# Optimization experiments

Hardware: AMD Instinct MI355X
Metric: run time of the kernel (lower is better)

The kernel has to match this reference:

```python
import jax, jax.numpy as jnp
import numpy as np
from jax import lax

D_MODEL = 512
D_STATE = 16
D_CONV = 4
EXPAND = 2
D_INNER = EXPAND * D_MODEL
DT_RANK = (D_MODEL + 15) // 16  # 32


def _mamba_dir(x, in_w, conv_w, conv_b, xproj_w, dt_w, dt_b, A_log, D, out_w):
    # x: (B, L, d_model)
    B, L, _ = x.shape
    xz = jnp.einsum('bld,ed->ble', x, in_w)          # (B, L, 2*d_inner)
    xi, z = jnp.split(xz, 2, axis=-1)                # each (B, L, d_inner)
    # causal depthwise conv over time
    xc = xi.transpose(0, 2, 1)                       # (B, d_inner, L)
    xc = lax.conv_general_dilated(
        xc, conv_w, window_strides=(1,), padding=[(D_CONV - 1, 0)],
        feature_group_count=D_INNER, dimension_numbers=('NCH', 'OIH', 'NCH'))
    xi = jax.nn.silu(xc + conv_b[None, :, None]).transpose(0, 2, 1)  # (B, L, d_inner)
    # input-dependent SSM params
    x_dbl = jnp.einsum('bld,ed->ble', xi, xproj_w)   # (B, L, dt_rank + 2*d_state)
    dt, Bc, Cc = jnp.split(x_dbl, [DT_RANK, DT_RANK + D_STATE], axis=-1)
    delta = jax.nn.softplus(jnp.einsum('blr,dr->bld', dt, dt_w) + dt_b)  # (B, L, d_inner)
    A = -jnp.exp(A_log)                              # (d_inner, d_state)
    deltaA = jnp.exp(delta[..., None] * A)           # (B, L, d_inner, d_state)
    dBx = delta[..., None] * Bc[:, :, None, :] * xi[..., None]  # (B, L, d_inner, d_state)

    def step(h, inputs):
        dA_t, dBx_t, C_t = inputs
        h = dA_t * h + dBx_t                         # (B, d_inner, d_state)
        y = jnp.einsum('bdn,bn->bd', h, C_t)
        return h, y

    h0 = jnp.zeros((B, D_INNER, D_STATE), dtype=x.dtype)
    _, ys = lax.scan(step, h0,
                     (deltaA.transpose(1, 0, 2, 3),
                      dBx.transpose(1, 0, 2, 3),
                      Cc.transpose(1, 0, 2)))
    y = ys.transpose(1, 0, 2)                        # (B, L, d_inner)
    y = y + xi * D
    y = y * jax.nn.silu(z)
    return jnp.einsum('ble,de->bld', y, out_w)       # (B, L, d_model)


def _forward(x, f_in_w, f_conv_w, f_conv_b, f_xproj_w, f_dt_w, f_dt_b, f_A_log, f_D, f_out_w,
             b_in_w, b_conv_w, b_conv_b, b_xproj_w, b_dt_w, b_dt_b, b_A_log, b_D, b_out_w,
             fusion_w, fusion_b, ln_g, ln_b):
    out_fwd = _mamba_dir(x, f_in_w, f_conv_w, f_conv_b, f_xproj_w, f_dt_w, f_dt_b, f_A_log, f_D, f_out_w)
    x_flip = jnp.flip(x, axis=1)
    out_bwd = _mamba_dir(x_flip, b_in_w, b_conv_w, b_conv_b, b_xproj_w, b_dt_w, b_dt_b, b_A_log, b_D, b_out_w)
    out_bwd = jnp.flip(out_bwd, axis=1)
    fused = jnp.concatenate([out_fwd, out_bwd], axis=-1)     # (B, L, 2*d_model)
    out = jnp.einsum('blf,df->bld', fused, fusion_w) + fusion_b
    r = x + out
    mu = jnp.mean(r, axis=-1, keepdims=True)
    var = jnp.var(r, axis=-1, keepdims=True)
    return (r - mu) * lax.rsqrt(var + 1e-5) * ln_g + ln_b


def _mamba_params(key):
    ks = jax.random.split(key, 6)
    s = 0.02
    in_w = jax.random.normal(ks[0], (2 * D_INNER, D_MODEL), jnp.float32) * s
    conv_w = jax.random.normal(ks[1], (D_INNER, 1, D_CONV), jnp.float32) * 0.2
    conv_b = jnp.zeros((D_INNER,), jnp.float32)
    xproj_w = jax.random.normal(ks[2], (DT_RANK + 2 * D_STATE, D_INNER), jnp.float32) * s
    dt_w = jax.random.normal(ks[3], (D_INNER, DT_RANK), jnp.float32) * (DT_RANK ** -0.5)
    dt_b = jax.random.uniform(ks[4], (D_INNER,), jnp.float32, -4.0, -2.0)
    A_log = jnp.log(jnp.broadcast_to(jnp.arange(1, D_STATE + 1, dtype=jnp.float32), (D_INNER, D_STATE)))
    D = jnp.ones((D_INNER,), jnp.float32)
    out_w = jax.random.normal(ks[5], (D_MODEL, D_INNER), jnp.float32) * s
    return in_w, conv_w, conv_b, xproj_w, dt_w, dt_b, A_log, D, out_w


def setup_inputs() -> dict:
    key = jax.random.key(0)
    kx, kf, kb, k1, k2 = jax.random.split(key, 5)
    B, L = 2, 1024
    x = jax.random.normal(kx, (B, L, D_MODEL), jnp.float32)
    f = _mamba_params(kf)
    b = _mamba_params(kb)
    fusion_w = jax.random.normal(k1, (D_MODEL, 2 * D_MODEL), jnp.float32) * 0.02
    fusion_b = jnp.zeros((D_MODEL,), jnp.float32)
    ln_g = jnp.ones((D_MODEL,), jnp.float32)
    ln_b = jnp.zeros((D_MODEL,), jnp.float32)
    names_f = ['f_in_w', 'f_conv_w', 'f_conv_b', 'f_xproj_w', 'f_dt_w', 'f_dt_b', 'f_A_log', 'f_D', 'f_out_w']
    names_b = ['b_in_w', 'b_conv_w', 'b_conv_b', 'b_xproj_w', 'b_dt_w', 'b_dt_b', 'b_A_log', 'b_D', 'b_out_w']
    d = {'x': x, 'fusion_w': fusion_w, 'fusion_b': fusion_b, 'ln_g': ln_g, 'ln_b': ln_b}
    d.update(dict(zip(names_f, f)))
    d.update(dict(zip(names_b, b)))
    return d


def reference(x, f_in_w, f_conv_w, f_conv_b, f_xproj_w, f_dt_w, f_dt_b, f_A_log, f_D, f_out_w,
              b_in_w, b_conv_w, b_conv_b, b_xproj_w, b_dt_w, b_dt_b, b_A_log, b_D, b_out_w,
              fusion_w, fusion_b, ln_g, ln_b):
    return _forward(x, f_in_w, f_conv_w, f_conv_b, f_xproj_w, f_dt_w, f_dt_b, f_A_log, f_D, f_out_w,
                    b_in_w, b_conv_w, b_conv_b, b_xproj_w, b_dt_w, b_dt_b, b_A_log, b_D, b_out_w,
                    fusion_w, fusion_b, ln_g, ln_b)
```

## Files before the change

### kernel.cpp

```cpp
#include <hip/hip_runtime.h>
#include <hip/hip_bf16.h>

typedef __bf16 bf16x8 __attribute__((ext_vector_type(8)));
typedef __bf16 bf16x4 __attribute__((ext_vector_type(4)));
typedef float  f32x4  __attribute__((ext_vector_type(4)));

#define LOG2E 1.44269504088896340f

static __device__ __forceinline__ unsigned short f2bf_bits(float f) {
  unsigned u = __builtin_bit_cast(unsigned, f);
  u = u + 0x7FFFu + ((u >> 16) & 1u);
  return (unsigned short)(u >> 16);
}
static __device__ __forceinline__ __bf16 to_bf16(float f) {
  unsigned short s = f2bf_bits(f);
  return __builtin_bit_cast(__bf16, s);
}
static __device__ __forceinline__ float fast_sigmoid(float x) {
  return __builtin_amdgcn_rcpf(1.f + __builtin_amdgcn_exp2f(-LOG2E * x));
}

struct CastSeg { const float* src; __bf16* dst; int n4; };
struct CastArgs { CastSeg s[8]; };

__global__ __launch_bounds__(256) void cast_kernel(CastArgs a) {
  CastSeg seg = a.s[blockIdx.y];
  int idx = blockIdx.x * 256 + threadIdx.x;
  int stride = gridDim.x * 256;
  const float4* src = (const float4*)seg.src;
  bf16x4* dst = (bf16x4*)seg.dst;
  for (int i = idx; i < seg.n4; i += stride) {
    float4 v = src[i];
    bf16x4 o;
    o[0] = to_bf16(v.x); o[1] = to_bf16(v.y);
    o[2] = to_bf16(v.z); o[3] = to_bf16(v.w);
    dst[i] = o;
  }
}

template<typename OutT, bool BIAS, bool RESID, bool SILUHI>
__global__ __launch_bounds__(256) void gemm_bt(
    const __bf16* __restrict__ A, long long sAz,
    const __bf16* __restrict__ B0, const __bf16* __restrict__ B1,
    OutT* __restrict__ C, long long sCz, int ldc,
    int N, int K,
    const float* __restrict__ bias, const float* __restrict__ resid, int ldr,
    int siluFrom)
{
  const __bf16* B = (blockIdx.z == 0) ? B0 : B1;
  A += (size_t)blockIdx.z * (size_t)sAz;
  C += (size_t)blockIdx.z * (size_t)sCz;
  int lane = threadIdx.x & 63;
  int wid  = threadIdx.x >> 6;
  int rowBase = blockIdx.y * 128 + (wid >> 1) * 64;
  int colBase = blockIdx.x * 128 + (wid & 1) * 64;
  int lr = lane & 15;
  int lk = (lane >> 4) << 3;
  const __bf16* Ap = A + (size_t)(rowBase + lr) * K + lk;
  const __bf16* Bp[4];
  #pragma unroll
  for (int ni = 0; ni < 4; ++ni) {
    int br = colBase + ni * 16 + lr;
    if (br > N - 1) br = N - 1;
    Bp[ni] = B + (size_t)br * K + lk;
  }
  f32x4 acc[4][4] = {};
  #pragma unroll 2
  for (int k = 0; k < K; k += 32) {
    bf16x8 aF[4], bF[4];
    #pragma unroll
    for (int mi = 0; mi < 4; ++mi)
      aF[mi] = *(const bf16x8*)(Ap + (size_t)(mi * 16) * K + k);
    #pragma unroll
    for (int ni = 0; ni < 4; ++ni)
      bF[ni] = *(const bf16x8*)(Bp[ni] + k);
    #pragma unroll
    for (int mi = 0; mi < 4; ++mi)
      #pragma unroll
      for (int ni = 0; ni < 4; ++ni)
        acc[mi][ni] = __builtin_amdgcn_mfma_f32_16x16x32_bf16(aF[mi], bF[ni], acc[mi][ni], 0, 0, 0);
  }
  int crow = rowBase + ((lane >> 4) << 2);
  int ccol = colBase + lr;
  #pragma unroll
  for (int mi = 0; mi < 4; ++mi) {
    #pragma unroll
    for (int ni = 0; ni < 4; ++ni) {
      int c = ccol + ni * 16;
      if (c < N) {
        #pragma unroll
        for (int j = 0; j < 4; ++j) {
          int r = crow + mi * 16 + j;
          float v = acc[mi][ni][j];
          if (BIAS)  v += bias[c];
          if (RESID) v += resid[(size_t)r * ldr + c];
          if (SILUHI && c >= siluFrom) v = v * fast_sigmoid(v);
          if constexpr (sizeof(OutT) == 2) C[(size_t)r * ldc + c] = to_bf16(v);
          else                             C[(size_t)r * ldc + c] = v;
        }
      }
    }
  }
}

#define CT 16
__global__ __launch_bounds__(256) void conv_silu_kernel(
    const float* __restrict__ xz,
    const float* __restrict__ f_cw, const float* __restrict__ f_cb,
    const float* __restrict__ b_cw, const float* __restrict__ b_cb,
    float* __restrict__ xi32,
    __bf16* __restrict__ xi16)
{
  int d  = blockIdx.x * 256 + threadIdx.x;
  int t0 = blockIdx.y * CT;
  int dir = blockIdx.z >> 1, b = blockIdx.z & 1;
  const float* cw = dir ? b_cw : f_cw;
  const float* cb = dir ? b_cb : f_cb;
  float w0 = cw[d*4+0], w1 = cw[d*4+1], w2 = cw[d*4+2], w3 = cw[d*4+3];
  float bias = cb[d];
  size_t rowBase = (size_t)dir * 2048 + (size_t)b * 1024;
  const float* xp = xz + rowBase * 2048 + d;
  float* o32 = xi32 + rowBase * 1024 + d;
  __bf16* o16 = xi16 + rowBase * 1024 + d;
  float xv[CT + 3];
  if (dir == 0) {
    #pragma unroll
    for (int j = 0; j < CT + 3; ++j) {
      int t = t0 - 3 + j;
      xv[j] = (t >= 0) ? xp[(size_t)t * 2048] : 0.f;
    }
    #pragma unroll
    for (int j = 0; j < CT; ++j) {
      int t = t0 + j;
      float v = fmaf(w0, xv[j], fmaf(w1, xv[j+1], fmaf(w2, xv[j+2], fmaf(w3, xv[j+3], bias))));
      float s = v * fast_sigmoid(v);
      o32[(size_t)t * 1024] = s;
      o16[(size_t)t * 1024] = to_bf16(s);
    }
  } else {
    #pragma unroll
    for (int j = 0; j < CT + 3; ++j) {
      int t = t0 + j;
      xv[j] = (t < 1024) ? xp[(size_t)t * 2048] : 0.f;
    }
    #pragma unroll
    for (int j = 0; j < CT; ++j) {
      int t = t0 + j;
      float v = fmaf(w3, xv[j], fmaf(w2, xv[j+1], fmaf(w1, xv[j+2], fmaf(w0, xv[j+3], bias))));
      float s = v * fast_sigmoid(v);
      o32[(size_t)t * 1024] = s;
      o16[(size_t)t * 1024] = to_bf16(s);
    }
  }
}

#define PR 16
__global__ __launch_bounds__(256) void prep_kernel(
    const float* __restrict__ xz,
    const float* __restrict__ xi32,
    const float* __restrict__ xdbl,
    const float* __restrict__ f_dtw, const float* __restrict__ f_dtb,
    const float* __restrict__ b_dtw, const float* __restrict__ b_dtb,
    const float* __restrict__ f_D, const float* __restrict__ b_D,
    float2* __restrict__ packA,
    float2* __restrict__ packB)
{
  int d = blockIdx.x * 256 + threadIdx.x;
  int dir = blockIdx.z;
  const float* dtw = dir ? b_dtw : f_dtw;
  const float* dtb = dir ? b_dtb : f_dtb;
  float Dv = (dir ? b_D : f_D)[d];
  float w[32];
  #pragma unroll
  for (int k = 0; k < 32; ++k) w[k] = dtw[d * 32 + k];
  float bias = dtb[d];
  int row0 = dir * 2048 + blockIdx.y * PR;
  #pragma unroll
  for (int r = 0; r < PR; ++r) {
    int row = row0 + r;
    const float4* xr = (const float4*)(xdbl + (size_t)row * 64);
    float acc = bias;
    #pragma unroll
    for (int q = 0; q < 8; ++q) {
      float4 v = xr[q];
      acc = fmaf(w[q*4+0], v.x, acc);
      acc = fmaf(w[q*4+1], v.y, acc);
      acc = fmaf(w[q*4+2], v.z, acc);
      acc = fmaf(w[q*4+3], v.w, acc);
    }
    float m = fmaxf(acc, 0.f);
    float e = __builtin_amdgcn_exp2f(-LOG2E * fabsf(acc));
    float del = fmaf(__builtin_amdgcn_logf(1.f + e), 1.f / LOG2E, m);
    float xi = xi32[(size_t)row * 1024 + d];
    float gate = xz[(size_t)row * 2048 + 1024 + d];
    packA[(size_t)row * 1024 + d] = float2{del, del * xi};
    packB[(size_t)row * 1024 + d] = float2{xi * Dv * gate, gate};
  }
}

#define NC 64
#define CL 16

__global__ __launch_bounds__(256) void scan_part1(
    const float2* __restrict__ packA,
    const float* __restrict__ xdbl,
    const float* __restrict__ f_Alog, const float* __restrict__ b_Alog,
    float4* __restrict__ aProd, float4* __restrict__ hPart)
{
  int d = blockIdx.x * 256 + threadIdx.x;
  int g = blockIdx.y;
  int zb = blockIdx.z;
  int dir = zb >> 1, b = zb & 1;
  const float* Alog = (dir ? b_Alog : f_Alog) + d * 16;
  float As[16];
  #pragma unroll
  for (int n = 0; n < 16; ++n)
    As[n] = -__builtin_amdgcn_exp2f(LOG2E * Alog[n]) * LOG2E;
  int base = dir * 2048 + b * 1024;
  float h[16], A[16];
  #pragma unroll
  for (int n = 0; n < 16; ++n) { h[n] = 0.f; A[n] = 1.f; }
  #pragma unroll
  for (int j = 0; j < CL; ++j) {
    int tau = g * CL + j;
    int row = base + (dir ? (1023 - tau) : tau);
    float2 v = packA[(size_t)row * 1024 + d];
    const float* xr = xdbl + (size_t)row * 64;
    #pragma unroll
    for (int n = 0; n < 16; ++n) {
      float Bv = xr[32 + n];
      float dA = __builtin_amdgcn_exp2f(v.x * As[n]);
      h[n] = fmaf(dA, h[n], v.y * Bv);
      A[n] *= dA;
    }
  }
  size_t o = (((size_t)zb * NC + g) * 1024 + d) * 4;
  #pragma unroll
  for (int q = 0; q < 4; ++q) {
    aProd[o + q] = float4{A[q*4+0], A[q*4+1], A[q*4+2], A[q*4+3]};
    hPart[o + q] = float4{h[q*4+0], h[q*4+1], h[q*4+2], h[q*4+3]};
  }
}

__global__ __launch_bounds__(256) void scan_combine(
    const float* __restrict__ aProd, const float* __restrict__ hPart,
    float* __restrict__ hIn)
{
  int idx = blockIdx.x * 256 + threadIdx.x;
  int zb = idx >> 14;
  int dn = idx & 16383;
  float H = 0.f;
  #pragma unroll 8
  for (int g = 0; g < NC; ++g) {
    size_t o = ((size_t)zb * NC + g) * 16384 + dn;
    float a = aProd[o];
    float hp = hPart[o];
    hIn[o] = H;
    H = fmaf(a, H, hp);
  }
}

__global__ __launch_bounds__(256) void scan_part3(
    const float2* __restrict__ packA, const float2* __restrict__ packB,
    const float* __restrict__ xdbl,
    const float* __restrict__ f_Alog, const float* __restrict__ b_Alog,
    const float* __restrict__ hIn,
    __bf16* __restrict__ yout)
{
  int d = blockIdx.x * 256 + threadIdx.x;
  int g = blockIdx.y;
  int zb = blockIdx.z;
  int dir = zb >> 1, b = zb & 1;
  const float* Alog = (dir ? b_Alog : f_Alog) + d * 16;
  float As[16];
  #pragma unroll
  for (int n = 0; n < 16; ++n)
    As[n] = -__builtin_amdgcn_exp2f(LOG2E * Alog[n]) * LOG2E;
  float h[16];
  const float4* hi4 = (const float4*)(hIn + (((size_t)zb * NC + g) * 1024 + d) * 16);
  #pragma unroll
  for (int q = 0; q < 4; ++q) {
    float4 hv = hi4[q];
    h[q*4+0] = hv.x; h[q*4+1] = hv.y; h[q*4+2] = hv.z; h[q*4+3] = hv.w;
  }
  int base = dir * 2048 + b * 1024;
  #pragma unroll
  for (int j = 0; j < CL; ++j) {
    int tau = g * CL + j;
    int row = base + (dir ? (1023 - tau) : tau);
    float2 v  = packA[(size_t)row * 1024 + d];
    float2 zw = packB[(size_t)row * 1024 + d];
    const float* xr = xdbl + (size_t)row * 64;
    float ps = 0.f;
    #pragma unroll
    for (int n = 0; n < 16; ++n) {
      float Bv = xr[32 + n];
      float Cv = xr[48 + n];
      float dA = __builtin_amdgcn_exp2f(v.x * As[n]);
      h[n] = fmaf(dA, h[n], v.y * Bv);
      ps = fmaf(h[n], Cv, ps);
    }
    float y = fmaf(ps, zw.y, zw.x);
    yout[(size_t)row * 1024 + d] = to_bf16(y);
  }
}

__global__ __launch_bounds__(256) void ln_kernel(
    const float* __restrict__ r, const float* __restrict__ g,
    const float* __restrict__ beta, float* __restrict__ out)
{
  int row = blockIdx.x;
  int tid = threadIdx.x;
  const float* rp = r + (size_t)row * 512;
  float v0 = rp[tid], v1 = rp[tid + 256];
  float s = v0 + v1;
  float q = fmaf(v0, v0, v1 * v1);
  #pragma unroll
  for (int m = 1; m < 64; m <<= 1) {
    s += __shfl_xor(s, m, 64);
    q += __shfl_xor(q, m, 64);
  }
  __shared__ float ls[4], lq[4];
  int wid = tid >> 6;
  if ((tid & 63) == 0) { ls[wid] = s; lq[wid] = q; }
  __syncthreads();
  s = ls[0] + ls[1] + ls[2] + ls[3];
  q = lq[0] + lq[1] + lq[2] + lq[3];
  float mu = s * (1.f / 512.f);
  float var = q * (1.f / 512.f) - mu * mu;
  float rs = rsqrtf(var + 1e-5f);
  float* op = out + (size_t)row * 512;
  op[tid]       = (v0 - mu) * rs * g[tid]       + beta[tid];
  op[tid + 256] = (v1 - mu) * rs * g[tid + 256] + beta[tid + 256];
}

extern "C" void kernel_launch(void* const* d_in, const int* in_sizes, int n_in,
                              void* d_out, int out_size, void* d_ws, size_t ws_size,
                              hipStream_t stream)
{
  const float* x        = (const float*)d_in[0];
  const float* fusion_w = (const float*)d_in[1];
  const float* fusion_b = (const float*)d_in[2];
  const float* ln_g     = (const float*)d_in[3];
  const float* ln_b     = (const float*)d_in[4];
  const float* f_in_w   = (const float*)d_in[5];
  const float* f_conv_w = (const float*)d_in[6];
  const float* f_conv_b = (const float*)d_in[7];
  const float* f_xproj  = (const float*)d_in[8];
  const float* f_dt_w   = (const float*)d_in[9];
  const float* f_dt_b   = (const float*)d_in[10];
  const float* f_A_log  = (const float*)d_in[11];
  const float* f_D      = (const float*)d_in[12];
  const float* f_out_w  = (const float*)d_in[13];
  const float* b_in_w   = (const float*)d_in[14];
  const float* b_conv_w = (const float*)d_in[15];
  const float* b_conv_b = (const float*)d_in[16];
  const float* b_xproj  = (const float*)d_in[17];
  const float* b_dt_w   = (const float*)d_in[18];
  const float* b_dt_b   = (const float*)d_in[19];
  const float* b_A_log  = (const float*)d_in[20];
  const float* b_D      = (const float*)d_in[21];
  const float* b_out_w  = (const float*)d_in[22];

  char* w = (char*)d_ws;
  auto alloc = [&](size_t bytes) -> char* {
    char* p = w;
    w += (bytes + 255) & ~(size_t)255;
    return p;
  };
  __bf16* xbf   = (__bf16*)alloc((size_t)2048 * 512 * 2);
  __bf16* wInF  = (__bf16*)alloc((size_t)2048 * 512 * 2);
  __bf16* wInB  = (__bf16*)alloc((size_t)2048 * 512 * 2);
  __bf16* xprF  = (__bf16*)alloc((size_t)64 * 1024 * 2);
  __bf16* xprB  = (__bf16*)alloc((size_t)64 * 1024 * 2);
  __bf16* wOutF = (__bf16*)alloc((size_t)512 * 1024 * 2);
  __bf16* wOutB = (__bf16*)alloc((size_t)512 * 1024 * 2);
  __bf16* wFus  = (__bf16*)alloc((size_t)512 * 1024 * 2);
  float*  xzbuf = (float*)alloc((size_t)2 * 2048 * 2048 * 4);
  float*  xi32  = (float*)alloc((size_t)2 * 2048 * 1024 * 4);
  __bf16* xi16  = (__bf16*)alloc((size_t)2 * 2048 * 1024 * 2);
  float*  xdbl  = (float*)alloc((size_t)2 * 2048 * 64 * 4);
  float2* packA = (float2*)alloc((size_t)4096 * 1024 * 8);
  float2* packB = (float2*)alloc((size_t)4096 * 1024 * 8);
  __bf16* ybf   = (__bf16*)alloc((size_t)2 * 2048 * 1024 * 2);
  __bf16* fin   = (__bf16*)alloc((size_t)2048 * 1024 * 2);
  float*  rbuf  = (float*)alloc((size_t)2048 * 512 * 4);
  float*  aProd = (float*)alloc((size_t)4 * NC * 16384 * 4);
  float*  hPart = (float*)alloc((size_t)4 * NC * 16384 * 4);
  float*  hInB  = (float*)alloc((size_t)4 * NC * 16384 * 4);
  (void)ws_size; (void)n_in; (void)in_sizes; (void)out_size;

  CastArgs ca;
  ca.s[0] = { x,        xbf,   (2048 * 512) / 4 };
  ca.s[1] = { f_in_w,   wInF,  (2048 * 512) / 4 };
  ca.s[2] = { b_in_w,   wInB,  (2048 * 512) / 4 };
  ca.s[3] = { f_xproj,  xprF,  (64 * 1024) / 4 };
  ca.s[4] = { b_xproj,  xprB,  (64 * 1024) / 4 };
  ca.s[5] = { f_out_w,  wOutF, (512 * 1024) / 4 };
  ca.s[6] = { b_out_w,  wOutB, (512 * 1024) / 4 };
  ca.s[7] = { fusion_w, wFus,  (512 * 1024) / 4 };
  cast_kernel<<<dim3(256, 8), 256, 0, stream>>>(ca);

  gemm_bt<float, false, false, true><<<dim3(16, 16, 2), 256, 0, stream>>>(
      xbf, 0LL, wInF, wInB, xzbuf, (long long)2048 * 2048, 2048, 2048, 512,
      nullptr, nullptr, 0, 1024);

  conv_silu_kernel<<<dim3(4, 1024 / CT, 4), 256, 0, stream>>>(
      xzbuf, f_conv_w, f_conv_b, b_conv_w, b_conv_b, xi32, xi16);

  gemm_bt<float, false, false, false><<<dim3(1, 16, 2), 256, 0, stream>>>(
      xi16, (long long)2048 * 1024, xprF, xprB, xdbl, (long long)2048 * 64, 64,
      64, 1024, nullptr, nullptr, 0, 0);

  prep_kernel<<<dim3(4, 2048 / PR, 2), 256, 0, stream>>>(
      xzbuf, xi32, xdbl, f_dt_w, f_dt_b, b_dt_w, b_dt_b, f_D, b_D,
      packA, packB);

  scan_part1<<<dim3(4, NC, 4), 256, 0, stream>>>(
      packA, xdbl, f_A_log, b_A_log, (float4*)aProd, (float4*)hPart);
  scan_combine<<<dim3(256), 256, 0, stream>>>(aProd, hPart, hInB);
  scan_part3<<<dim3(4, NC, 4), 256, 0, stream>>>(
      packA, packB, xdbl, f_A_log, b_A_log, hInB, ybf);

  gemm_bt<__bf16, false, false, false><<<dim3(4, 16, 2), 256, 0, stream>>>(
      ybf, (long long)2048 * 1024, wOutF, wOutB, fin, 512LL, 1024, 512, 1024,
      nullptr, nullptr, 0, 0);

  gemm_bt<float, true, true, false><<<dim3(4, 16, 1), 256, 0, stream>>>(
      fin, 0LL, wFus, wFus, rbuf, 0LL, 512, 512, 1024,
      fusion_b, x, 512, 0);

  ln_kernel<<<2048, 256, 0, stream>>>(rbuf, ln_g, ln_b, (float*)d_out);
}
```

Baseline: 317.9 us.

## Fuse delta/softplus into scan kernels, split in-proj output, split-K x_proj GEMM

Removes prep_kernel and its packA/packB buffers. The scan kernels now recompute the dt projection and softplus per timestep from xdbl and xi32 instead of reading packed float2 arrays. The in-proj GEMM epilogue writes xi as fp32 and the silu gate as bf16 into separate compact buffers, cutting intermediate traffic. The small-N x_proj GEMM is replaced by a split-K kernel with a reduction pass to raise parallelism. The cost is that the delta computation runs twice, once in each scan pass, adding ALU work and extra launches.

```diff
diff --git a/kernel.cpp b/kernel.cpp
--- a/kernel.cpp
+++ b/kernel.cpp
@@ -18,6 +18,11 @@
 }
 static __device__ __forceinline__ float fast_sigmoid(float x) {
   return __builtin_amdgcn_rcpf(1.f + __builtin_amdgcn_exp2f(-LOG2E * x));
+}
+static __device__ __forceinline__ float softplus_f(float x) {
+  float m = fmaxf(x, 0.f);
+  float e = __builtin_amdgcn_exp2f(-LOG2E * fabsf(x));
+  return fmaf(__builtin_amdgcn_logf(1.f + e), 1.f / LOG2E, m);
 }
 
 struct CastSeg { const float* src; __bf16* dst; int n4; };
@@ -38,18 +43,22 @@
   }
 }
 
-template<typename OutT, bool BIAS, bool RESID, bool SILUHI>
+template<typename OutT, bool BIAS, bool RESID, bool SPLIT>
 __global__ __launch_bounds__(256) void gemm_bt(
     const __bf16* __restrict__ A, long long sAz,
     const __bf16* __restrict__ B0, const __bf16* __restrict__ B1,
     OutT* __restrict__ C, long long sCz, int ldc,
     int N, int K,
     const float* __restrict__ bias, const float* __restrict__ resid, int ldr,
-    int siluFrom)
+    float* __restrict__ xiout, __bf16* __restrict__ gateout, long long sXz)
 {
   const __bf16* B = (blockIdx.z == 0) ? B0 : B1;
   A += (size_t)blockIdx.z * (size_t)sAz;
   C += (size_t)blockIdx.z * (size_t)sCz;
+  if (SPLIT) {
+    xiout  += (size_t)blockIdx.z * (size_t)sXz;
+    gateout += (size_t)blockIdx.z * (size_t)sXz;
+  }
   int lane = threadIdx.x & 63;
   int wid  = threadIdx.x >> 6;
   int rowBase = blockIdx.y * 128 + (wid >> 1) * 64;
@@ -92,11 +101,16 @@
         for (int j = 0; j < 4; ++j) {
           int r = crow + mi * 16 + j;
           float v = acc[mi][ni][j];
-          if (BIAS)  v += bias[c];
-          if (RESID) v += resid[(size_t)r * ldr + c];
-          if (SILUHI && c >= siluFrom) v = v * fast_sigmoid(v);
-          if constexpr (sizeof(OutT) == 2) C[(size_t)r * ldc + c] = to_bf16(v);
-          else                             C[(size_t)r * ldc + c] = v;
+          if (SPLIT) {
+            if (c < 1024) xiout[(size_t)r * 1024 + c] = v;
+            else          gateout[(size_t)r * 1024 + (c - 1024)] =
+                              to_bf16(v * fast_sigmoid(v));
+          } else {
+            if (BIAS)  v += bias[c];
+            if (RESID) v += resid[(size_t)r * ldr + c];
+            if constexpr (sizeof(OutT) == 2) C[(size_t)r * ldc + c] = to_bf16(v);
+            else                             C[(size_t)r * ldc + c] = v;
+          }
         }
       }
     }
@@ -105,7 +119,7 @@
 
 #define CT 16
 __global__ __launch_bounds__(256) void conv_silu_kernel(
-    const float* __restrict__ xz,
+    const float* __restrict__ xiraw,
     const float* __restrict__ f_cw, const float* __restrict__ f_cb,
     const float* __restrict__ b_cw, const float* __restrict__ b_cb,
     float* __restrict__ xi32,
@@ -119,7 +133,7 @@
   float w0 = cw[d*4+0], w1 = cw[d*4+1], w2 = cw[d*4+2], w3 = cw[d*4+3];
   float bias = cb[d];
   size_t rowBase = (size_t)dir * 2048 + (size_t)b * 1024;
-  const float* xp = xz + rowBase * 2048 + d;
+  const float* xp = xiraw + rowBase * 1024 + d;
   float* o32 = xi32 + rowBase * 1024 + d;
   __bf16* o16 = xi16 + rowBase * 1024 + d;
   float xv[CT + 3];
@@ -127,7 +141,7 @@
     #pragma unroll
     for (int j = 0; j < CT + 3; ++j) {
       int t = t0 - 3 + j;
-      xv[j] = (t >= 0) ? xp[(size_t)t * 2048] : 0.f;
+      xv[j] = (t >= 0) ? xp[(size_t)t * 1024] : 0.f;
     }
     #pragma unroll
     for (int j = 0; j < CT; ++j) {
@@ -141,7 +155,7 @@
     #pragma unroll
     for (int j = 0; j < CT + 3; ++j) {
       int t = t0 + j;
-      xv[j] = (t < 1024) ? xp[(size_t)t * 2048] : 0.f;
+      xv[j] = (t < 1024) ? xp[(size_t)t * 1024] : 0.f;
     }
     #pragma unroll
     for (int j = 0; j < CT; ++j) {
@@ -154,56 +168,68 @@
   }
 }
 
-#define PR 16
-__global__ __launch_bounds__(256) void prep_kernel(
-    const float* __restrict__ xz,
+__global__ __launch_bounds__(256) void g2_kernel(
+    const __bf16* __restrict__ A,
+    const __bf16* __restrict__ B0, const __bf16* __restrict__ B1,
+    float* __restrict__ partial)
+{
+  int slice = blockIdx.x;
+  int mt = blockIdx.y;
+  int dir = blockIdx.z;
+  const __bf16* B = dir ? B1 : B0;
+  const __bf16* Ad = A + (size_t)dir * 2048 * 1024;
+  int lane = threadIdx.x & 63, wid = threadIdx.x >> 6;
+  int rowBase = mt * 64 + wid * 16;
+  int lr = lane & 15, lk = (lane >> 4) << 3;
+  int k0 = slice * 256;
+  const __bf16* Ap = Ad + (size_t)(rowBase + lr) * 1024 + k0 + lk;
+  const __bf16* Bp[4];
+  #pragma unroll
+  for (int ni = 0; ni < 4; ++ni)
+    Bp[ni] = B + (size_t)(ni * 16 + lr) * 1024 + k0 + lk;
+  f32x4 acc[4] = {};
+  #pragma unroll
+  for (int k = 0; k < 256; k += 32) {
+    bf16x8 aF = *(const bf16x8*)(Ap + k);
+    #pragma unroll
+    for (int ni = 0; ni < 4; ++ni) {
+      bf16x8 bF = *(const bf16x8*)(Bp[ni] + k);
+      acc[ni] = __builtin_amdgcn_mfma_f32_16x16x32_bf16(aF, bF, acc[ni], 0, 0, 0);
+    }
+  }
+  int crow = rowBase + ((lane >> 4) << 2);
+  float* out = partial + ((size_t)dir * 4 + slice) * 2048 * 64;
+  #pragma unroll
+  for (int ni = 0; ni < 4; ++ni)
+    #pragma unroll
+    for (int j = 0; j < 4; ++j)
+      out[(size_t)(crow + j) * 64 + ni * 16 + lr] = acc[ni][j];
+}
+
+__global__ __launch_bounds__(256) void g2red_kernel(
+    const float4* __restrict__ partial, float4* __restrict__ xdbl)
+{
+  int idx = blockIdx.x * 256 + threadIdx.x;
+  int dir = idx >> 15;
+  int rest = idx & 32767;
+  const float4* p = partial + (size_t)dir * 4 * 32768 + rest;
+  float4 a = p[0], b = p[32768], c = p[2 * 32768], d = p[3 * 32768];
+  float4 s;
+  s.x = a.x + b.x + c.x + d.x;
+  s.y = a.y + b.y + c.y + d.y;
+  s.z = a.z + b.z + c.z + d.z;
+  s.w = a.w + b.w + c.w + d.w;
+  xdbl[idx] = s;
+}
+
+#define NC 64
+#define CL 16
+
+__global__ __launch_bounds__(256) void scan_part1(
     const float* __restrict__ xi32,
     const float* __restrict__ xdbl,
     const float* __restrict__ f_dtw, const float* __restrict__ f_dtb,
     const float* __restrict__ b_dtw, const float* __restrict__ b_dtb,
-    const float* __restrict__ f_D, const float* __restrict__ b_D,
-    float2* __restrict__ packA,
-    float2* __restrict__ packB)
-{
-  int d = blockIdx.x * 256 + threadIdx.x;
-  int dir = blockIdx.z;
-  const float* dtw = dir ? b_dtw : f_dtw;
-  const float* dtb = dir ? b_dtb : f_dtb;
-  float Dv = (dir ? b_D : f_D)[d];
-  float w[32];
-  #pragma unroll
-  for (int k = 0; k < 32; ++k) w[k] = dtw[d * 32 + k];
-  float bias = dtb[d];
-  int row0 = dir * 2048 + blockIdx.y * PR;
-  #pragma unroll
-  for (int r = 0; r < PR; ++r) {
-    int row = row0 + r;
-    const float4* xr = (const float4*)(xdbl + (size_t)row * 64);
-    float acc = bias;
-    #pragma unroll
-    for (int q = 0; q < 8; ++q) {
-      float4 v = xr[q];
-      acc = fmaf(w[q*4+0], v.x, acc);
-      acc = fmaf(w[q*4+1], v.y, acc);
-      acc = fmaf(w[q*4+2], v.z, acc);
-      acc = fmaf(w[q*4+3], v.w, acc);
-    }
-    float m = fmaxf(acc, 0.f);
-    float e = __builtin_amdgcn_exp2f(-LOG2E * fabsf(acc));
-    float del = fmaf(__builtin_amdgcn_logf(1.f + e), 1.f / LOG2E, m);
-    float xi = xi32[(size_t)row * 1024 + d];
-    float gate = xz[(size_t)row * 2048 + 1024 + d];
-    packA[(size_t)row * 1024 + d] = float2{del, del * xi};
-    packB[(size_t)row * 1024 + d] = float2{xi * Dv * gate, gate};
-  }
-}
-
-#define NC 64
-#define CL 16
-
-__global__ __launch_bounds__(256) void scan_part1(
-    const float2* __restrict__ packA,
-    const float* __restrict__ xdbl,
     const float* __restrict__ f_Alog, const float* __restrict__ b_Alog,
     float4* __restrict__ aProd, float4* __restrict__ hPart)
 {
@@ -211,6 +237,11 @@
   int g = blockIdx.y;
   int zb = blockIdx.z;
   int dir = zb >> 1, b = zb & 1;
+  const float* dtw = (dir ? b_dtw : f_dtw) + d * 32;
+  float w[32];
+  #pragma unroll
+  for (int k = 0; k < 32; ++k) w[k] = dtw[k];
+  float dtb = (dir ? b_dtb : f_dtb)[d];
   const float* Alog = (dir ? b_Alog : f_Alog) + d * 16;
   float As[16];
   #pragma unroll
@@ -224,13 +255,17 @@
   for (int j = 0; j < CL; ++j) {
     int tau = g * CL + j;
     int row = base + (dir ? (1023 - tau) : tau);
-    float2 v = packA[(size_t)row * 1024 + d];
     const float* xr = xdbl + (size_t)row * 64;
+    float acc = dtb;
+    #pragma unroll
+    for (int k = 0; k < 32; ++k) acc = fmaf(w[k], xr[k], acc);
+    float del = softplus_f(acc);
+    float xi = xi32[(size_t)row * 1024 + d];
+    float dx = del * xi;
     #pragma unroll
     for (int n = 0; n < 16; ++n) {
-      float Bv = xr[32 + n];
-      float dA = __builtin_amdgcn_exp2f(v.x * As[n]);
-      h[n] = fmaf(dA, h[n], v.y * Bv);
+      float dA = __builtin_amdgcn_exp2f(del * As[n]);
+      h[n] = fmaf(dA, h[n], dx * xr[32 + n]);
       A[n] *= dA;
     }
   }
@@ -261,9 +296,13 @@
 }
 
 __global__ __launch_bounds__(256) void scan_part3(
-    const float2* __restrict__ packA, const float2* __restrict__ packB,
+    const float* __restrict__ xi32,
     const float* __restrict__ xdbl,
+    const __bf16* __restrict__ gatebf,
+    const float* __restrict__ f_dtw, const float* __restrict__ f_dtb,
+    const float* __restrict__ b_dtw, const float* __restrict__ b_dtb,
     const float* __restrict__ f_Alog, const float* __restrict__ b_Alog,
+    const float* __restrict__ f_D, const float* __restrict__ b_D,
     const float* __restrict__ hIn,
     __bf16* __restrict__ yout)
 {
@@ -271,6 +310,12 @@
   int g = blockIdx.y;
   int zb = blockIdx.z;
   int dir = zb >> 1, b = zb & 1;
+  const float* dtw = (dir ? b_dtw : f_dtw) + d * 32;
+  float w[32];
+  #pragma unroll
+  for (int k = 0; k < 32; ++k) w[k] = dtw[k];
+  float dtb = (dir ? b_dtb : f_dtb)[d];
+  float Dv = (dir ? b_D : f_D)[d];
   const float* Alog = (dir ? b_Alog : f_Alog) + d * 16;
   float As[16];
   #pragma unroll
@@ -288,19 +333,22 @@
   for (int j = 0; j < CL; ++j) {
     int tau = g * CL + j;
     int row = base + (dir ? (1023 - tau) : tau);
-    float2 v  = packA[(size_t)row * 1024 + d];
-    float2 zw = packB[(size_t)row * 1024 + d];
     const float* xr = xdbl + (size_t)row * 64;
+    float acc = dtb;
+    #pragma unroll
+    for (int k = 0; k < 32; ++k) acc = fmaf(w[k], xr[k], acc);
+    float del = softplus_f(acc);
+    float xi = xi32[(size_t)row * 1024 + d];
+    float dx = del * xi;
     float ps = 0.f;
     #pragma unroll
     for (int n = 0; n < 16; ++n) {
-      float Bv = xr[32 + n];
-      float Cv = xr[48 + n];
-      float dA = __builtin_amdgcn_exp2f(v.x * As[n]);
-      h[n] = fmaf(dA, h[n], v.y * Bv);
-      ps = fmaf(h[n], Cv, ps);
-    }
-    float y = fmaf(ps, zw.y, zw.x);
+      float dA = __builtin_amdgcn_exp2f(del * As[n]);
+      h[n] = fmaf(dA, h[n], dx * xr[32 + n]);
+      ps = fmaf(h[n], xr[48 + n], ps);
+    }
+    float gate = (float)gatebf[(size_t)row * 1024 + d];
+    float y = fmaf(xi, Dv, ps) * gate;
     yout[(size_t)row * 1024 + d] = to_bf16(y);
   }
 }
@@ -368,26 +416,26 @@
     w += (bytes + 255) & ~(size_t)255;
     return p;
   };
-  __bf16* xbf   = (__bf16*)alloc((size_t)2048 * 512 * 2);
-  __bf16* wInF  = (__bf16*)alloc((size_t)2048 * 512 * 2);
-  __bf16* wInB  = (__bf16*)alloc((size_t)2048 * 512 * 2);
-  __bf16* xprF  = (__bf16*)alloc((size_t)64 * 1024 * 2);
-  __bf16* xprB  = (__bf16*)alloc((size_t)64 * 1024 * 2);
-  __bf16* wOutF = (__bf16*)alloc((size_t)512 * 1024 * 2);
-  __bf16* wOutB = (__bf16*)alloc((size_t)512 * 1024 * 2);
-  __bf16* wFus  = (__bf16*)alloc((size_t)512 * 1024 * 2);
-  float*  xzbuf = (float*)alloc((size_t)2 * 2048 * 2048 * 4);
-  float*  xi32  = (float*)alloc((size_t)2 * 2048 * 1024 * 4);
-  __bf16* xi16  = (__bf16*)alloc((size_t)2 * 2048 * 1024 * 2);
-  float*  xdbl  = (float*)alloc((size_t)2 * 2048 * 64 * 4);
-  float2* packA = (float2*)alloc((size_t)4096 * 1024 * 8);
-  float2* packB = (float2*)alloc((size_t)4096 * 1024 * 8);
-  __bf16* ybf   = (__bf16*)alloc((size_t)2 * 2048 * 1024 * 2);
-  __bf16* fin   = (__bf16*)alloc((size_t)2048 * 1024 * 2);
-  float*  rbuf  = (float*)alloc((size_t)2048 * 512 * 4);
-  float*  aProd = (float*)alloc((size_t)4 * NC * 16384 * 4);
-  float*  hPart = (float*)alloc((size_t)4 * NC * 16384 * 4);
-  float*  hInB  = (float*)alloc((size_t)4 * NC * 16384 * 4);
+  __bf16* xbf    = (__bf16*)alloc((size_t)2048 * 512 * 2);
+  __bf16* wInF   = (__bf16*)alloc((size_t)2048 * 512 * 2);
+  __bf16* wInB   = (__bf16*)alloc((size_t)2048 * 512 * 2);
+  __bf16* xprF   = (__bf16*)alloc((size_t)64 * 1024 * 2);
+  __bf16* xprB   = (__bf16*)alloc((size_t)64 * 1024 * 2);
+  __bf16* wOutF  = (__bf16*)alloc((size_t)512 * 1024 * 2);
+  __bf16* wOutB  = (__bf16*)alloc((size_t)512 * 1024 * 2);
+  __bf16* wFus   = (__bf16*)alloc((size_t)512 * 1024 * 2);
+  float*  xiraw  = (float*)alloc((size_t)2 * 2048 * 1024 * 4);
+  __bf16* gatebf = (__bf16*)alloc((size_t)2 * 2048 * 1024 * 2);
+  float*  xi32   = (float*)alloc((size_t)2 * 2048 * 1024 * 4);
+  __bf16* xi16   = (__bf16*)alloc((size_t)2 * 2048 * 1024 * 2);
+  float*  part2  = (float*)alloc((size_t)2 * 4 * 2048 * 64 * 4);
+  float*  xdbl   = (float*)alloc((size_t)2 * 2048 * 64 * 4);
+  __bf16* ybf    = (__bf16*)alloc((size_t)2 * 2048 * 1024 * 2);
+  __bf16* fin    = (__bf16*)alloc((size_t)2048 * 1024 * 2);
+  float*  rbuf   = (float*)alloc((size_t)2048 * 512 * 4);
+  float*  aProd  = (float*)alloc((size_t)4 * NC * 16384 * 4);
+  float*  hPart  = (float*)alloc((size_t)4 * NC * 16384 * 4);
+  float*  hInB   = (float*)alloc((size_t)4 * NC * 16384 * 4);
   (void)ws_size; (void)n_in; (void)in_sizes; (void)out_size;
 
   CastArgs ca;
@@ -402,33 +450,30 @@
   cast_kernel<<<dim3(256, 8), 256, 0, stream>>>(ca);
 
   gemm_bt<float, false, false, true><<<dim3(16, 16, 2), 256, 0, stream>>>(
-      xbf, 0LL, wInF, wInB, xzbuf, (long long)2048 * 2048, 2048, 2048, 512,
-      nullptr, nullptr, 0, 1024);
+      xbf, 0LL, wInF, wInB, (float*)nullptr, 0LL, 0, 2048, 512,
+      nullptr, nullptr, 0, xiraw, gatebf, (long long)2048 * 1024);
 
   conv_silu_kernel<<<dim3(4, 1024 / CT, 4), 256, 0, stream>>>(
-      xzbuf, f_conv_w, f_conv_b, b_conv_w, b_conv_b, xi32, xi16);
-
-  gemm_bt<float, false, false, false><<<dim3(1, 16, 2), 256, 0, stream>>>(
-      xi16, (long long)2048 * 1024, xprF, xprB, xdbl, (long long)2048 * 64, 64,
-      64, 1024, nullptr, nullptr, 0, 0);
-
-  prep_kernel<<<dim3(4, 2048 / PR, 2), 256, 0, stream>>>(
-      xzbuf, xi32, xdbl, f_dt_w, f_dt_b, b_dt_w, b_dt_b, f_D, b_D,
-      packA, packB);
+      xiraw, f_conv_w, f_conv_b, b_conv_w, b_conv_b, xi32, xi16);
+
+  g2_kernel<<<dim3(4, 32, 2), 256, 0, stream>>>(xi16, xprF, xprB, part2);
+  g2red_kernel<<<dim3(256), 256, 0, stream>>>((const float4*)part2, (float4*)xdbl);
 
   scan_part1<<<dim3(4, NC, 4), 256, 0, stream>>>(
-      packA, xdbl, f_A_log, b_A_log, (float4*)aProd, (float4*)hPart);
+      xi32, xdbl, f_dt_w, f_dt_b, b_dt_w, b_dt_b, f_A_log, b_A_log,
+      (float4*)aProd, (float4*)hPart);
   scan_combine<<<dim3(256), 256, 0, stream>>>(aProd, hPart, hInB);
   scan_part3<<<dim3(4, NC, 4), 256, 0, stream>>>(
-      packA, packB, xdbl, f_A_log, b_A_log, hInB, ybf);
+      xi32, xdbl, gatebf, f_dt_w, f_dt_b, b_dt_w, b_dt_b, f_A_log, b_A_log,
+      f_D, b_D, hInB, ybf);
 
   gemm_bt<__bf16, false, false, false><<<dim3(4, 16, 2), 256, 0, stream>>>(
       ybf, (long long)2048 * 1024, wOutF, wOutB, fin, 512LL, 1024, 512, 1024,
-      nullptr, nullptr, 0, 0);
+      nullptr, nullptr, 0, nullptr, nullptr, 0LL);
 
   gemm_bt<float, true, true, false><<<dim3(4, 16, 1), 256, 0, stream>>>(
       fin, 0LL, wFus, wFus, rbuf, 0LL, 512, 512, 1024,
-      fusion_b, x, 512, 0);
+      fusion_b, x, 512, nullptr, nullptr, 0LL);
 
   ln_kernel<<<2048, 256, 0, stream>>>(rbuf, ln_g, ln_b, (float*)d_out);
 }
```

New measurement: 310.6 us. 2.3% less time.
